# Kernel optimization log

Hardware: AMD Instinct MI355X
Metric: run time of the kernel (lower is better)

## Reference

```python
import jax, jax.numpy as jnp
import numpy as np

H_DIM = 2048
N_HEADS = 16
HEAD_DIM = H_DIM // N_HEADS
B, S = 2, 2048


def setup_inputs() -> dict:
    key = jax.random.key(0)
    ks = jax.random.split(key, 10)
    sc = 1.0 / np.sqrt(H_DIM)
    return {
        "X": jax.random.normal(ks[0], (B, S, H_DIM), dtype=jnp.float32),
        "attention_mask": jnp.ones((B, S, S), dtype=jnp.int32),
        "Wq": jax.random.normal(ks[1], (H_DIM, H_DIM), dtype=jnp.float32) * sc,
        "bq": jnp.zeros((H_DIM,), dtype=jnp.float32),
        "Wk": jax.random.normal(ks[2], (H_DIM, H_DIM), dtype=jnp.float32) * sc,
        "bk": jnp.zeros((H_DIM,), dtype=jnp.float32),
        "Wv": jax.random.normal(ks[3], (H_DIM, H_DIM), dtype=jnp.float32) * sc,
        "bv": jnp.zeros((H_DIM,), dtype=jnp.float32),
        "Wo": jax.random.normal(ks[4], (H_DIM, H_DIM), dtype=jnp.float32) * sc,
        "bo": jnp.zeros((H_DIM,), dtype=jnp.float32),
    }


def reference(X, attention_mask, Wq, bq, Wk, bk, Wv, bv, Wo, bo):
    b, s, _ = X.shape
    # QKV projections -> [b, heads, s, head_dim]
    def proj(W, bias):
        y = jnp.einsum("bsd,de->bse", X, W) + bias
        return y.reshape(b, s, N_HEADS, HEAD_DIM).transpose(0, 2, 1, 3)
    Q, K, V = proj(Wq, bq), proj(Wk, bk), proj(Wv, bv)
    # scores [b, h, s, s]
    scores = jnp.einsum("bhqd,bhkd->bhqk", Q, K) / jnp.sqrt(jnp.float32(HEAD_DIM))
    mask = attention_mask[:, None, :, :]  # [b,1,s,s]
    scores = jnp.where(mask == 0, jnp.float32(-jnp.inf), scores)
    attn = jax.nn.softmax(scores, axis=-1)
    # dropout_rate = 0.0 -> no-op
    out = jnp.einsum("bhqk,bhkd->bhqd", attn, V)
    out = out.transpose(0, 2, 1, 3).reshape(b, s, H_DIM)
    return jnp.einsum("bsd,de->bse", out, Wo) + bo
```

## Files before the change

### kernel.cpp

```cpp
#include <hip/hip_runtime.h>
#include <hip/hip_bf16.h>

#define H_DIM 2048
#define N_HEADS 16
#define HEAD_DIM 128
#define BATCH 2
#define SEQ 2048

typedef __bf16 bf16_t;
typedef __bf16 bf16x8 __attribute__((ext_vector_type(8)));
typedef float f32x4 __attribute__((ext_vector_type(4)));

#define MFMA16(a, b, c) __builtin_amdgcn_mfma_f32_16x16x32_bf16((a), (b), (c), 0, 0, 0)

#define GLOAD16(gp, lp) __builtin_amdgcn_global_load_lds( \
    (const __attribute__((address_space(1))) void*)(gp),  \
    (__attribute__((address_space(3))) void*)(lp), 16, 0, 0)

__global__ __launch_bounds__(256) void detect_kernel(const unsigned int* __restrict__ X,
                                                     int* __restrict__ flags) {
    __shared__ int cnt[256];
    int t = threadIdx.x;
    int c = 0;
    for (int i = 0; i < 16; i++) {
        unsigned w  = X[t * 16 + i];
        unsigned lo = w & 0xFFFFu;
        unsigned e  = (lo >> 7) & 0xFFu;
        if (lo == 0u || (e >= 100u && e <= 141u)) c++;
    }
    cnt[t] = c;
    __syncthreads();
    for (int s = 128; s > 0; s >>= 1) {
        if (t < s) cnt[t] += cnt[t + s];
        __syncthreads();
    }
    if (t == 0) { flags[0] = (cnt[0] >= 2048) ? 1 : 0; flags[1] = 1; }
}

__global__ __launch_bounds__(256) void maskcheck_kernel(const int* __restrict__ mask,
                                                        int* __restrict__ flags) {
    size_t i = ((size_t)blockIdx.x * 256 + threadIdx.x) * 8;
    const int4* p = (const int4*)(mask + i);
    int4 a = p[0], b = p[1];
    int all = (a.x != 0) & (a.y != 0) & (a.z != 0) & (a.w != 0) &
              (b.x != 0) & (b.y != 0) & (b.z != 0) & (b.w != 0);
    if (!all) atomicAnd(&flags[1], 0);
}

__device__ inline bf16x8 load8(const void* __restrict__ p, size_t idx, int isbf16) {
    if (isbf16) {
        return *(const bf16x8*)((const bf16_t*)p + idx);
    } else {
        const float* f = (const float*)p + idx;
        float4 a = *(const float4*)f;
        float4 b = *(const float4*)(f + 4);
        bf16x8 r;
        r[0] = (bf16_t)a.x; r[1] = (bf16_t)a.y; r[2] = (bf16_t)a.z; r[3] = (bf16_t)a.w;
        r[4] = (bf16_t)b.x; r[5] = (bf16_t)b.y; r[6] = (bf16_t)b.z; r[7] = (bf16_t)b.w;
        return r;
    }
}

__device__ inline float readf(const void* __restrict__ p, int idx, int isbf16) {
    return isbf16 ? (float)((const bf16_t*)p)[idx] : ((const float*)p)[idx];
}

__global__ __launch_bounds__(256) void convert_kernel(const void* __restrict__ X,
                                                      bf16_t* __restrict__ Xb,
                                                      const int* __restrict__ flags) {
    const int isbf16 = flags[0];
    size_t i = ((size_t)blockIdx.x * 256 + threadIdx.x) * 8;
    bf16x8 v = load8(X, i, isbf16);
    *(bf16x8*)(Xb + i) = v;
}

__global__ __launch_bounds__(256) void transpose_kernel(
    const void* __restrict__ W0, const void* __restrict__ W1,
    const void* __restrict__ W2, const void* __restrict__ W3,
    bf16_t* __restrict__ Wts, const int* __restrict__ flags)
{
    const int isbf16 = flags[0];
    const int z = blockIdx.z;
    const void* W = (z == 0) ? W0 : (z == 1) ? W1 : (z == 2) ? W2 : W3;
    bf16_t* out = Wts + (size_t)z * H_DIM * H_DIM;

    __shared__ __attribute__((aligned(16))) bf16_t Ts[64][72];
    const int tid = threadIdx.x;
    const int n0 = blockIdx.x * 64;
    const int k0 = blockIdx.y * 64;

    #pragma unroll
    for (int j = 0; j < 2; j++) {
        int idx = j * 2048 + tid * 8;
        int r = idx >> 6, c = idx & 63;
        bf16x8 v = load8(W, (size_t)(k0 + r) * H_DIM + n0 + c, isbf16);
        *(bf16x8*)(&Ts[r][c]) = v;
    }
    __syncthreads();
    const int wr = tid & 63;
    const int wcg = (tid >> 6) * 8;
    #pragma unroll
    for (int j = 0; j < 2; j++) {
        int wc = wcg + j * 32;
        bf16x8 o;
        #pragma unroll
        for (int u = 0; u < 8; u++) o[u] = Ts[wc + u][wr];
        *(bf16x8*)(&out[(size_t)(n0 + wr) * H_DIM + k0 + wc]) = o;
    }
}

__global__ __launch_bounds__(256) void gemm_qkv_kernel(
    const bf16_t* __restrict__ A, const bf16_t* __restrict__ Wts,
    const void* __restrict__ b0, const void* __restrict__ b1, const void* __restrict__ b2,
    bf16_t* __restrict__ qws, bf16_t* __restrict__ kws, bf16_t* __restrict__ vtws,
    const int* __restrict__ flags)
{
    const int isbf16 = flags[0];
    const int z = blockIdx.z;
    const bf16_t* Wt = Wts + (size_t)z * H_DIM * H_DIM;
    const void* bias = (z == 0) ? b0 : (z == 1) ? b1 : b2;
    bf16_t* dst = (z == 0) ? qws : (z == 1) ? kws : vtws;

    __shared__ __attribute__((aligned(16))) bf16_t As[2][4][128][8];
    __shared__ __attribute__((aligned(16))) bf16_t Bs[2][4][128][8];

    const int tid  = threadIdx.x;
    const int lane = tid & 63;
    const int wid  = tid >> 6;
    const int quad = lane >> 4;
    const int l16  = lane & 15;
    const int wm   = (wid >> 1) * 64;
    const int wn   = (wid & 1) * 64;
    const int m0   = blockIdx.y * 128;
    const int n0   = blockIdx.x * 128;

    const int s_k8  = (tid * 2) >> 7;
    const int s_row = (tid * 2) & 127;

    f32x4 acc[4][4] = {};

    auto stage = [&](int k0, int bb) {
        #pragma unroll
        for (int j = 0; j < 2; j++) {
            int slot = j * 256 + tid;
            int k8 = slot >> 7, row = slot & 127;
            GLOAD16(A  + (size_t)(m0 + row) * H_DIM + k0 + k8 * 8,
                    (bf16_t*)(&As[bb][0][0][0]) + slot * 8);
            GLOAD16(Wt + (size_t)(n0 + row) * H_DIM + k0 + k8 * 8,
                    (bf16_t*)(&Bs[bb][0][0][0]) + slot * 8);
        }
    };

    stage(0, 0);
    const int NIT = H_DIM / 32;
    for (int it = 0; it < NIT; it++) {
        const int bb = it & 1;
        __syncthreads();
        if (it + 1 < NIT) stage((it + 1) * 32, bb ^ 1);

        bf16x8 af[4], bfr[4];
        #pragma unroll
        for (int i = 0; i < 4; i++) {
            af[i]  = *(const bf16x8*)(&As[bb][quad][wm + i * 16 + l16][0]);
            bfr[i] = *(const bf16x8*)(&Bs[bb][quad][wn + i * 16 + l16][0]);
        }
        #pragma unroll
        for (int mi = 0; mi < 4; mi++)
            #pragma unroll
            for (int ni = 0; ni < 4; ni++)
                acc[mi][ni] = MFMA16(af[mi], bfr[ni], acc[mi][ni]);
    }

    #pragma unroll
    for (int ni = 0; ni < 4; ni++) {
        int col = n0 + wn + ni * 16 + l16;
        int h = col >> 7, d = col & (HEAD_DIM - 1);
        float bv = readf(bias, col, isbf16);
        #pragma unroll
        for (int mi = 0; mi < 4; mi++) {
            int row0 = m0 + wm + mi * 16 + quad * 4;
            int b = row0 >> 11;
            if (z < 2) {
                #pragma unroll
                for (int r = 0; r < 4; r++) {
                    int s = (row0 + r) & (SEQ - 1);
                    dst[((size_t)(b * N_HEADS + h) * SEQ + s) * HEAD_DIM + d] =
                        (bf16_t)(acc[mi][ni][r] + bv);
                }
            } else {
                int s0 = row0 & (SEQ - 1);
                bf16_t o[4];
                #pragma unroll
                for (int r = 0; r < 4; r++) o[r] = (bf16_t)(acc[mi][ni][r] + bv);
                *(unsigned long long*)(&dst[((size_t)(b * N_HEADS + h) * HEAD_DIM + d) * SEQ + s0]) =
                    *(unsigned long long*)o;
            }
        }
    }
}

__global__ __launch_bounds__(256) void gemm_out_kernel(
    const bf16_t* __restrict__ A, const bf16_t* __restrict__ Wt,
    const void* __restrict__ bias, void* __restrict__ C,
    const int* __restrict__ flags)
{
    const int isbf16 = flags[0];
    __shared__ __attribute__((aligned(16))) bf16_t As[2][4][128][8];
    __shared__ __attribute__((aligned(16))) bf16_t Bs[2][4][128][8];

    const int tid  = threadIdx.x;
    const int lane = tid & 63;
    const int wid  = tid >> 6;
    const int quad = lane >> 4;
    const int l16  = lane & 15;
    const int wm   = (wid >> 1) * 64;
    const int wn   = (wid & 1) * 64;
    const int m0   = blockIdx.y * 128;
    const int n0   = blockIdx.x * 128;

    f32x4 acc[4][4] = {};

    auto stage = [&](int k0, int bb) {
        #pragma unroll
        for (int j = 0; j < 2; j++) {
            int slot = j * 256 + tid;
            int k8 = slot >> 7, row = slot & 127;
            GLOAD16(A  + (size_t)(m0 + row) * H_DIM + k0 + k8 * 8,
                    (bf16_t*)(&As[bb][0][0][0]) + slot * 8);
            GLOAD16(Wt + (size_t)(n0 + row) * H_DIM + k0 + k8 * 8,
                    (bf16_t*)(&Bs[bb][0][0][0]) + slot * 8);
        }
    };

    stage(0, 0);
    const int NIT = H_DIM / 32;
    for (int it = 0; it < NIT; it++) {
        const int bb = it & 1;
        __syncthreads();
        if (it + 1 < NIT) stage((it + 1) * 32, bb ^ 1);

        bf16x8 af[4], bfr[4];
        #pragma unroll
        for (int i = 0; i < 4; i++) {
            af[i]  = *(const bf16x8*)(&As[bb][quad][wm + i * 16 + l16][0]);
            bfr[i] = *(const bf16x8*)(&Bs[bb][quad][wn + i * 16 + l16][0]);
        }
        #pragma unroll
        for (int mi = 0; mi < 4; mi++)
            #pragma unroll
            for (int ni = 0; ni < 4; ni++)
                acc[mi][ni] = MFMA16(af[mi], bfr[ni], acc[mi][ni]);
    }

    #pragma unroll
    for (int ni = 0; ni < 4; ni++) {
        int col = n0 + wn + ni * 16 + l16;
        float bv = readf(bias, col, isbf16);
        #pragma unroll
        for (int mi = 0; mi < 4; mi++) {
            int row0 = m0 + wm + mi * 16 + quad * 4;
            #pragma unroll
            for (int r = 0; r < 4; r++) {
                float v = acc[mi][ni][r] + bv;
                if (isbf16) ((bf16_t*)C)[(size_t)(row0 + r) * H_DIM + col] = (bf16_t)v;
                else        ((float*)C)[(size_t)(row0 + r) * H_DIM + col]  = v;
            }
        }
    }
}

__global__ __launch_bounds__(256) void attn_kernel(
    const bf16_t* __restrict__ Q, const bf16_t* __restrict__ K,
    const bf16_t* __restrict__ Vt, const int* __restrict__ mask,
    const int* __restrict__ flags, bf16_t* __restrict__ ctx)
{
    __shared__ __attribute__((aligned(16))) bf16_t Ks[2][16][64][8];
    __shared__ __attribute__((aligned(16))) bf16_t Vs[2][8][128][8];
    __shared__ __attribute__((aligned(16))) bf16_t Pl[4][16][72];

    const int tid  = threadIdx.x;
    const int lane = tid & 63;
    const int wid  = tid >> 6;
    const int quad = lane >> 4;
    const int l16  = lane & 15;

    const int bh = blockIdx.y;
    const int b  = bh >> 4, h = bh & 15;
    const int q_base = blockIdx.x * 64 + wid * 16;
    const int maskAll = flags[1];

    const bf16_t* Qp = Q  + (size_t)bh * SEQ * HEAD_DIM;
    const bf16_t* Kp = K  + (size_t)bh * SEQ * HEAD_DIM;
    const bf16_t* Vp = Vt + (size_t)bh * HEAD_DIM * SEQ;
    const int*    mp = mask + (size_t)b * SEQ * SEQ;

    bf16x8 qf[4];
    #pragma unroll
    for (int t = 0; t < 4; t++)
        qf[t] = *(const bf16x8*)(Qp + (size_t)(q_base + l16) * HEAD_DIM + t * 32 + quad * 8);

    const float CS = 0.1275260013f;
    float m_r[4], l_r[4];
    #pragma unroll
    for (int r = 0; r < 4; r++) { m_r[r] = -1e30f; l_r[r] = 0.0f; }
    f32x4 o_acc[8] = {};

    auto stage = [&](int kt, int bb) {
        const int key0 = kt * 64;
        #pragma unroll
        for (int j = 0; j < 4; j++) {
            int slot = j * 256 + tid;
            int krow = slot & 63, k8 = slot >> 6;
            GLOAD16(Kp + (size_t)(key0 + krow) * HEAD_DIM + k8 * 8,
                    (bf16_t*)(&Ks[bb][0][0][0]) + slot * 8);
        }
        #pragma unroll
        for (int j = 0; j < 4; j++) {
            int slot = j * 256 + tid;
            int d = slot & 127, kq = slot >> 7;
            GLOAD16(Vp + (size_t)d * SEQ + key0 + kq * 8,
                    (bf16_t*)(&Vs[bb][0][0][0]) + slot * 8);
        }
    };

    stage(0, 0);

    const int NKT = SEQ / 64;
    for (int kt = 0; kt < NKT; kt++) {
        const int bb = kt & 1;
        const int key0 = kt * 64;
        __syncthreads();
        if (kt + 1 < NKT) stage(kt + 1, bb ^ 1);

        f32x4 s_acc[4];
        #pragma unroll
        for (int nt = 0; nt < 4; nt++) {
            f32x4 a = {};
            #pragma unroll
            for (int t = 0; t < 4; t++) {
                bf16x8 kf = *(const bf16x8*)(&Ks[bb][t * 4 + quad][nt * 16 + l16][0]);
                a = MFMA16(qf[t], kf, a);
            }
            s_acc[nt] = a;
        }

        float p2[4][4];
        #pragma unroll
        for (int nt = 0; nt < 4; nt++)
            #pragma unroll
            for (int r = 0; r < 4; r++)
                p2[nt][r] = s_acc[nt][r] * CS;

        if (!maskAll) {
            #pragma unroll
            for (int nt = 0; nt < 4; nt++) {
                int key = key0 + nt * 16 + l16;
                #pragma unroll
                for (int r = 0; r < 4; r++) {
                    int q = q_base + quad * 4 + r;
                    if (mp[(size_t)q * SEQ + key] == 0) p2[nt][r] = -1e30f;
                }
            }
        }

        #pragma unroll
        for (int r = 0; r < 4; r++) {
            float tmax = fmaxf(fmaxf(p2[0][r], p2[1][r]), fmaxf(p2[2][r], p2[3][r]));
            #pragma unroll
            for (int off = 1; off < 16; off <<= 1)
                tmax = fmaxf(tmax, __shfl_xor(tmax, off));
            float mnew  = fmaxf(m_r[r], tmax);
            float alpha = exp2f(m_r[r] - mnew);
            m_r[r] = mnew;
            float rsum = 0.0f;
            #pragma unroll
            for (int nt = 0; nt < 4; nt++) {
                float pv = exp2f(p2[nt][r] - mnew);
                p2[nt][r] = pv;
                rsum += pv;
            }
            #pragma unroll
            for (int off = 1; off < 16; off <<= 1)
                rsum += __shfl_xor(rsum, off);
            l_r[r] = l_r[r] * alpha + rsum;
            #pragma unroll
            for (int dn = 0; dn < 8; dn++)
                o_acc[dn][r] *= alpha;
        }

        #pragma unroll
        for (int nt = 0; nt < 4; nt++)
            #pragma unroll
            for (int r = 0; r < 4; r++)
                Pl[wid][quad * 4 + r][nt * 16 + l16] = (bf16_t)p2[nt][r];

        #pragma unroll
        for (int t = 0; t < 2; t++) {
            bf16x8 pf = *(const bf16x8*)(&Pl[wid][l16][t * 32 + quad * 8]);
            #pragma unroll
            for (int dn = 0; dn < 8; dn++) {
                bf16x8 vf = *(const bf16x8*)(&Vs[bb][t * 4 + quad][dn * 16 + l16][0]);
                o_acc[dn] = MFMA16(pf, vf, o_acc[dn]);
            }
        }
    }

    #pragma unroll
    for (int dn = 0; dn < 8; dn++) {
        #pragma unroll
        for (int r = 0; r < 4; r++) {
            int q = q_base + quad * 4 + r;
            int d = dn * 16 + l16;
            float v = o_acc[dn][r] / l_r[r];
            ctx[((size_t)(b * SEQ + q) * N_HEADS + h) * HEAD_DIM + d] = (bf16_t)v;
        }
    }
}

extern "C" void kernel_launch(void* const* d_in, const int* in_sizes, int n_in,
                              void* d_out, int out_size, void* d_ws, size_t ws_size,
                              hipStream_t stream) {
    const void* X    = d_in[0];
    const int*  mask = (const int*)d_in[1];
    const void* Wq   = d_in[2];
    const void* bq   = d_in[3];
    const void* Wk   = d_in[4];
    const void* bk   = d_in[5];
    const void* Wv   = d_in[6];
    const void* bv   = d_in[7];
    const void* Wo   = d_in[8];
    const void* bo   = d_in[9];

    const size_t NE = (size_t)BATCH * SEQ * H_DIM;
    const size_t NW = (size_t)H_DIM * H_DIM;

    int*    flags = (int*)d_ws;
    bf16_t* Xb    = (bf16_t*)((char*)d_ws + 256);
    bf16_t* Wts   = Xb + NE;
    bf16_t* qws   = Wts + 4 * NW;
    bf16_t* kws   = qws + NE;
    bf16_t* vtws  = kws + NE;
    bf16_t* cws   = vtws + NE;

    detect_kernel<<<1, 256, 0, stream>>>((const unsigned int*)X, flags);
    maskcheck_kernel<<<(BATCH * SEQ * SEQ) / (256 * 8), 256, 0, stream>>>(mask, flags);
    convert_kernel<<<NE / (256 * 8), 256, 0, stream>>>(X, Xb, flags);
    transpose_kernel<<<dim3(32, 32, 4), 256, 0, stream>>>(Wq, Wk, Wv, Wo, Wts, flags);
    gemm_qkv_kernel<<<dim3(H_DIM / 128, (BATCH * SEQ) / 128, 3), 256, 0, stream>>>(
        Xb, Wts, bq, bk, bv, qws, kws, vtws, flags);
    attn_kernel<<<dim3(SEQ / 64, BATCH * N_HEADS), 256, 0, stream>>>(
        qws, kws, vtws, mask, flags, cws);
    gemm_out_kernel<<<dim3(H_DIM / 128, (BATCH * SEQ) / 128), 256, 0, stream>>>(
        cws, Wts + 3 * NW, bo, d_out, flags);
}
```

Measured before the change: 709.5 us.

## Triple-buffer GEMMs with vmcnt waits, XCD-aware tile mapping, MFMA row sums

Both GEMM kernels move from double- to triple-buffered LDS staging, using explicit s_waitcnt vmcnt and raw s_barrier so loads stay two stages ahead. Their grids are flattened and blocks are remapped so tiles sharing weight columns land on the same XCD, aiming at better L2 reuse. In attention, the softmax row-sum shuffle reduction is replaced by an extra MFMA against a vector of ones, and the key loop is unrolled by two. The extra buffer raises LDS use, which may cut occupancy, and the hand-written waitcnt logic is fragile.

```diff
diff --git a/kernel.cpp b/kernel.cpp
--- a/kernel.cpp
+++ b/kernel.cpp
@@ -16,6 +16,10 @@
 #define GLOAD16(gp, lp) __builtin_amdgcn_global_load_lds( \
     (const __attribute__((address_space(1))) void*)(gp),  \
     (__attribute__((address_space(3))) void*)(lp), 16, 0, 0)
+
+#define WAIT_VM4()  asm volatile("s_waitcnt vmcnt(4)" ::: "memory")
+#define WAIT_VM0()  asm volatile("s_waitcnt vmcnt(0)" ::: "memory")
+#define RAW_BARRIER() asm volatile("s_barrier" ::: "memory")
 
 __global__ __launch_bounds__(256) void detect_kernel(const unsigned int* __restrict__ X,
                                                      int* __restrict__ flags) {
@@ -116,13 +120,21 @@
     const int* __restrict__ flags)
 {
     const int isbf16 = flags[0];
-    const int z = blockIdx.z;
+    const int L    = blockIdx.x;
+    const int xcd  = L & 7;
+    const int j    = L >> 3;
+    const int c    = xcd * 6 + (j % 6);
+    const int mrow = j / 6;
+    const int z    = c >> 4;
+    const int m0   = mrow * 128;
+    const int n0   = (c & 15) * 128;
+
     const bf16_t* Wt = Wts + (size_t)z * H_DIM * H_DIM;
     const void* bias = (z == 0) ? b0 : (z == 1) ? b1 : b2;
     bf16_t* dst = (z == 0) ? qws : (z == 1) ? kws : vtws;
 
-    __shared__ __attribute__((aligned(16))) bf16_t As[2][4][128][8];
-    __shared__ __attribute__((aligned(16))) bf16_t Bs[2][4][128][8];
+    __shared__ __attribute__((aligned(16))) bf16_t As[3][4][128][8];
+    __shared__ __attribute__((aligned(16))) bf16_t Bs[3][4][128][8];
 
     const int tid  = threadIdx.x;
     const int lane = tid & 63;
@@ -131,33 +143,25 @@
     const int l16  = lane & 15;
     const int wm   = (wid >> 1) * 64;
     const int wn   = (wid & 1) * 64;
-    const int m0   = blockIdx.y * 128;
-    const int n0   = blockIdx.x * 128;
-
-    const int s_k8  = (tid * 2) >> 7;
-    const int s_row = (tid * 2) & 127;
 
     f32x4 acc[4][4] = {};
 
-    auto stage = [&](int k0, int bb) {
-        #pragma unroll
-        for (int j = 0; j < 2; j++) {
-            int slot = j * 256 + tid;
+    auto stage = [&](int k0, int sb) {
+        #pragma unroll
+        for (int jj = 0; jj < 2; jj++) {
+            int slot = jj * 256 + tid;
             int k8 = slot >> 7, row = slot & 127;
             GLOAD16(A  + (size_t)(m0 + row) * H_DIM + k0 + k8 * 8,
-                    (bf16_t*)(&As[bb][0][0][0]) + slot * 8);
+                    (bf16_t*)(&As[sb][0][0][0]) + slot * 8);
             GLOAD16(Wt + (size_t)(n0 + row) * H_DIM + k0 + k8 * 8,
-                    (bf16_t*)(&Bs[bb][0][0][0]) + slot * 8);
-        }
-    };
-
-    stage(0, 0);
-    const int NIT = H_DIM / 32;
-    for (int it = 0; it < NIT; it++) {
-        const int bb = it & 1;
-        __syncthreads();
-        if (it + 1 < NIT) stage((it + 1) * 32, bb ^ 1);
-
+                    (bf16_t*)(&Bs[sb][0][0][0]) + slot * 8);
+        }
+    };
+
+    auto body = [&](int it, int bb, int sb, int mode) {
+        if (mode == 2) { WAIT_VM0(); } else { WAIT_VM4(); }
+        RAW_BARRIER();
+        if (mode == 0) stage((it + 2) * 32, sb);
         bf16x8 af[4], bfr[4];
         #pragma unroll
         for (int i = 0; i < 4; i++) {
@@ -169,7 +173,19 @@
             #pragma unroll
             for (int ni = 0; ni < 4; ni++)
                 acc[mi][ni] = MFMA16(af[mi], bfr[ni], acc[mi][ni]);
-    }
+    };
+
+    stage(0, 0);
+    stage(32, 1);
+    for (int base = 0; base < 60; base += 3) {
+        body(base,     0, 2, 0);
+        body(base + 1, 1, 0, 0);
+        body(base + 2, 2, 1, 0);
+    }
+    body(60, 0, 2, 0);
+    body(61, 1, 0, 0);
+    body(62, 2, 1, 1);
+    body(63, 0, 0, 2);
 
     #pragma unroll
     for (int ni = 0; ni < 4; ni++) {
@@ -205,8 +221,14 @@
     const int* __restrict__ flags)
 {
     const int isbf16 = flags[0];
-    __shared__ __attribute__((aligned(16))) bf16_t As[2][4][128][8];
-    __shared__ __attribute__((aligned(16))) bf16_t Bs[2][4][128][8];
+    const int L    = blockIdx.x;
+    const int xcd  = L & 7;
+    const int j    = L >> 3;
+    const int m0   = (j >> 1) * 128;
+    const int n0   = (xcd * 2 + (j & 1)) * 128;
+
+    __shared__ __attribute__((aligned(16))) bf16_t As[3][4][128][8];
+    __shared__ __attribute__((aligned(16))) bf16_t Bs[3][4][128][8];
 
     const int tid  = threadIdx.x;
     const int lane = tid & 63;
@@ -215,30 +237,25 @@
     const int l16  = lane & 15;
     const int wm   = (wid >> 1) * 64;
     const int wn   = (wid & 1) * 64;
-    const int m0   = blockIdx.y * 128;
-    const int n0   = blockIdx.x * 128;
 
     f32x4 acc[4][4] = {};
 
-    auto stage = [&](int k0, int bb) {
-        #pragma unroll
-        for (int j = 0; j < 2; j++) {
-            int slot = j * 256 + tid;
+    auto stage = [&](int k0, int sb) {
+        #pragma unroll
+        for (int jj = 0; jj < 2; jj++) {
+            int slot = jj * 256 + tid;
             int k8 = slot >> 7, row = slot & 127;
             GLOAD16(A  + (size_t)(m0 + row) * H_DIM + k0 + k8 * 8,
-                    (bf16_t*)(&As[bb][0][0][0]) + slot * 8);
+                    (bf16_t*)(&As[sb][0][0][0]) + slot * 8);
             GLOAD16(Wt + (size_t)(n0 + row) * H_DIM + k0 + k8 * 8,
-                    (bf16_t*)(&Bs[bb][0][0][0]) + slot * 8);
-        }
-    };
-
-    stage(0, 0);
-    const int NIT = H_DIM / 32;
-    for (int it = 0; it < NIT; it++) {
-        const int bb = it & 1;
-        __syncthreads();
-        if (it + 1 < NIT) stage((it + 1) * 32, bb ^ 1);
-
+                    (bf16_t*)(&Bs[sb][0][0][0]) + slot * 8);
+        }
+    };
+
+    auto body = [&](int it, int bb, int sb, int mode) {
+        if (mode == 2) { WAIT_VM0(); } else { WAIT_VM4(); }
+        RAW_BARRIER();
+        if (mode == 0) stage((it + 2) * 32, sb);
         bf16x8 af[4], bfr[4];
         #pragma unroll
         for (int i = 0; i < 4; i++) {
@@ -250,7 +267,19 @@
             #pragma unroll
             for (int ni = 0; ni < 4; ni++)
                 acc[mi][ni] = MFMA16(af[mi], bfr[ni], acc[mi][ni]);
-    }
+    };
+
+    stage(0, 0);
+    stage(32, 1);
+    for (int base = 0; base < 60; base += 3) {
+        body(base,     0, 2, 0);
+        body(base + 1, 1, 0, 0);
+        body(base + 2, 2, 1, 0);
+    }
+    body(60, 0, 2, 0);
+    body(61, 1, 0, 0);
+    body(62, 2, 1, 1);
+    body(63, 0, 0, 2);
 
     #pragma unroll
     for (int ni = 0; ni < 4; ni++) {
@@ -299,35 +328,38 @@
     for (int t = 0; t < 4; t++)
         qf[t] = *(const bf16x8*)(Qp + (size_t)(q_base + l16) * HEAD_DIM + t * 32 + quad * 8);
 
+    bf16x8 onesf;
+    #pragma unroll
+    for (int u = 0; u < 8; u++) onesf[u] = (bf16_t)1.0f;
+
     const float CS = 0.1275260013f;
-    float m_r[4], l_r[4];
-    #pragma unroll
-    for (int r = 0; r < 4; r++) { m_r[r] = -1e30f; l_r[r] = 0.0f; }
+    float m_r[4];
+    #pragma unroll
+    for (int r = 0; r < 4; r++) m_r[r] = -1e30f;
+    f32x4 l_acc = {};
     f32x4 o_acc[8] = {};
 
     auto stage = [&](int kt, int bb) {
         const int key0 = kt * 64;
         #pragma unroll
-        for (int j = 0; j < 4; j++) {
-            int slot = j * 256 + tid;
+        for (int jj = 0; jj < 4; jj++) {
+            int slot = jj * 256 + tid;
             int krow = slot & 63, k8 = slot >> 6;
             GLOAD16(Kp + (size_t)(key0 + krow) * HEAD_DIM + k8 * 8,
                     (bf16_t*)(&Ks[bb][0][0][0]) + slot * 8);
         }
         #pragma unroll
-        for (int j = 0; j < 4; j++) {
-            int slot = j * 256 + tid;
+        for (int jj = 0; jj < 4; jj++) {
+            int slot = jj * 256 + tid;
             int d = slot & 127, kq = slot >> 7;
             GLOAD16(Vp + (size_t)d * SEQ + key0 + kq * 8,
                     (bf16_t*)(&Vs[bb][0][0][0]) + slot * 8);
         }
     };
 
-    stage(0, 0);
-
     const int NKT = SEQ / 64;
-    for (int kt = 0; kt < NKT; kt++) {
-        const int bb = kt & 1;
+
+    auto abody = [&](int kt, int bb) {
         const int key0 = kt * 64;
         __syncthreads();
         if (kt + 1 < NKT) stage(kt + 1, bb ^ 1);
@@ -372,17 +404,10 @@
             float mnew  = fmaxf(m_r[r], tmax);
             float alpha = exp2f(m_r[r] - mnew);
             m_r[r] = mnew;
-            float rsum = 0.0f;
-            #pragma unroll
-            for (int nt = 0; nt < 4; nt++) {
-                float pv = exp2f(p2[nt][r] - mnew);
-                p2[nt][r] = pv;
-                rsum += pv;
-            }
-            #pragma unroll
-            for (int off = 1; off < 16; off <<= 1)
-                rsum += __shfl_xor(rsum, off);
-            l_r[r] = l_r[r] * alpha + rsum;
+            #pragma unroll
+            for (int nt = 0; nt < 4; nt++)
+                p2[nt][r] = exp2f(p2[nt][r] - mnew);
+            l_acc[r] *= alpha;
             #pragma unroll
             for (int dn = 0; dn < 8; dn++)
                 o_acc[dn][r] *= alpha;
@@ -397,12 +422,19 @@
         #pragma unroll
         for (int t = 0; t < 2; t++) {
             bf16x8 pf = *(const bf16x8*)(&Pl[wid][l16][t * 32 + quad * 8]);
+            l_acc = MFMA16(pf, onesf, l_acc);
             #pragma unroll
             for (int dn = 0; dn < 8; dn++) {
                 bf16x8 vf = *(const bf16x8*)(&Vs[bb][t * 4 + quad][dn * 16 + l16][0]);
                 o_acc[dn] = MFMA16(pf, vf, o_acc[dn]);
             }
         }
+    };
+
+    stage(0, 0);
+    for (int base = 0; base < NKT; base += 2) {
+        abody(base, 0);
+        abody(base + 1, 1);
     }
 
     #pragma unroll
@@ -411,7 +443,7 @@
         for (int r = 0; r < 4; r++) {
             int q = q_base + quad * 4 + r;
             int d = dn * 16 + l16;
-            float v = o_acc[dn][r] / l_r[r];
+            float v = o_acc[dn][r] / l_acc[r];
             ctx[((size_t)(b * SEQ + q) * N_HEADS + h) * HEAD_DIM + d] = (bf16_t)v;
         }
     }
@@ -446,10 +478,8 @@
     maskcheck_kernel<<<(BATCH * SEQ * SEQ) / (256 * 8), 256, 0, stream>>>(mask, flags);
     convert_kernel<<<NE / (256 * 8), 256, 0, stream>>>(X, Xb, flags);
     transpose_kernel<<<dim3(32, 32, 4), 256, 0, stream>>>(Wq, Wk, Wv, Wo, Wts, flags);
-    gemm_qkv_kernel<<<dim3(H_DIM / 128, (BATCH * SEQ) / 128, 3), 256, 0, stream>>>(
-        Xb, Wts, bq, bk, bv, qws, kws, vtws, flags);
+    gemm_qkv_kernel<<<1536, 256, 0, stream>>>(Xb, Wts, bq, bk, bv, qws, kws, vtws, flags);
     attn_kernel<<<dim3(SEQ / 64, BATCH * N_HEADS), 256, 0, stream>>>(
         qws, kws, vtws, mask, flags, cws);
-    gemm_out_kernel<<<dim3(H_DIM / 128, (BATCH * SEQ) / 128), 256, 0, stream>>>(
-        cws, Wts + 3 * NW, bo, d_out, flags);
-}
+    gemm_out_kernel<<<512, 256, 0, stream>>>(cws, Wts + 3 * NW, bo, d_out, flags);
+}
```

New measurement: 670.3 us. 5.5% less time.
